# Kernel tuning notes

Hardware: AMD Instinct MI355X
Metric: run time of the kernel (lower is better)

Reference implementation:

```python
import jax, jax.numpy as jnp
import numpy as np

NUM_HEADS = 8
WINDOW = 64
ENCODERS = 6
EPS = 1e-5


def _positional_encoding(S, D, dtype=jnp.float32):
    pos = jnp.arange(S, dtype=jnp.float32)[:, None]
    div = jnp.exp(-jnp.log(10000.0) * jnp.arange(0, D, 2, dtype=jnp.float32) / D)
    ang = pos * div  # [S, D/2]
    pe = jnp.zeros((S, D), dtype=jnp.float32)
    pe = pe.at[:, 0::2].set(jnp.sin(ang)).at[:, 1::2].set(jnp.cos(ang))
    return pe.astype(dtype)


def _layernorm(x, g, b):
    mu = jnp.mean(x, axis=-1, keepdims=True)
    var = jnp.var(x, axis=-1, keepdims=True)
    return (x - mu) * jax.lax.rsqrt(var + EPS) * g + b


def _local_attention(x, wq, bq, wk, bk, wv, bv, window_mask):
    B, S, D = x.shape
    Dh = D // NUM_HEADS
    scale = Dh ** -0.5
    def split(t):  # [B,S,D] -> [B,H,S,Dh]
        return t.reshape(B, S, NUM_HEADS, Dh).transpose(0, 2, 1, 3)
    q = split(x @ wq.T + bq)
    k = split(x @ wk.T + bk)
    v = split(x @ wv.T + bv)
    scores = jnp.einsum('bhqd,bhkd->bhqk', q, k)
    # FAITHFUL: out-of-window entries are ZERO (not -inf); softmax over full S.
    scores = jnp.where(window_mask, scores, 0.0) * scale
    probs = jax.nn.softmax(scores, axis=-1)
    out = jnp.einsum('bhqk,bhkd->bhqd', probs, v)
    return out.transpose(0, 2, 1, 3).reshape(B, S, D)


def reference(inputs, emb, wq, bq, wk, bk, wv, bv, ln_g, ln_b,
              fc1_w, fc1_b, fc2_w, fc2_b, out_w, out_b):
    B, S = inputs.shape
    D = emb.shape[1]
    # window slice in torch source: [max(0, i-W), min(S, i+W))  (end exclusive)
    i = jnp.arange(S)[:, None]
    j = jnp.arange(S)[None, :]
    window_mask = (j >= i - WINDOW) & (j < i + WINDOW)  # [S, S]

    x = emb[inputs]  # [B, S, D]
    x = x + _positional_encoding(S, D, x.dtype)
    for _ in range(ENCODERS):  # shared weights across encoder iterations
        a = _local_attention(x, wq, bq, wk, bk, wv, bv, window_mask)
        x = _layernorm(a, ln_g, ln_b)
        h = jax.nn.relu(x @ fc1_w.T + fc1_b)
        x = (h @ fc2_w.T + fc2_b) + x
        x = _layernorm(x, ln_g, ln_b)
    x = x.reshape(B, S * D)
    return x @ out_w.T + out_b


def setup_inputs() -> dict:
    key = jax.random.key(0)
    ks = jax.random.split(key, 16)
    B, S, D, Hd, V, C = 8, 1024, 512, 2048, 32000, 6
    s = 0.02
    return {
        'inputs': jax.random.randint(ks[0], (B, S), 0, 31999),
        'emb': jax.random.normal(ks[1], (V, D), jnp.float32) * s,
        'wq': jax.random.normal(ks[2], (D, D), jnp.float32) * s,
        'bq': jnp.zeros((D,), jnp.float32),
        'wk': jax.random.normal(ks[3], (D, D), jnp.float32) * s,
        'bk': jnp.zeros((D,), jnp.float32),
        'wv': jax.random.normal(ks[4], (D, D), jnp.float32) * s,
        'bv': jnp.zeros((D,), jnp.float32),
        'ln_g': jnp.ones((D,), jnp.float32),
        'ln_b': jnp.zeros((D,), jnp.float32),
        'fc1_w': jax.random.normal(ks[5], (Hd, D), jnp.float32) * s,
        'fc1_b': jnp.zeros((Hd,), jnp.float32),
        'fc2_w': jax.random.normal(ks[6], (D, Hd), jnp.float32) * s,
        'fc2_b': jnp.zeros((D,), jnp.float32),
        'out_w': jax.random.normal(ks[7], (C, S * D), jnp.float32) * s,
        'out_b': jnp.zeros((C,), jnp.float32),
    }
```

## Files before the change

kernel.cpp:

```cpp
#include <hip/hip_runtime.h>

#define S_LEN 1024
#define DMODEL 512
#define NHEADS 8
#define DHEAD 64
#define HDIM 2048
#define WIN 64

typedef _Float16 f16x8 __attribute__((ext_vector_type(8)));
typedef _Float16 f16x2 __attribute__((ext_vector_type(2)));
typedef float f32x4 __attribute__((ext_vector_type(4)));
typedef float f32x16 __attribute__((ext_vector_type(16)));

__device__ __forceinline__ void stage16(const _Float16* g, _Float16* l) {
  __builtin_amdgcn_global_load_lds((const __attribute__((address_space(1))) unsigned int*)g,
                                   (__attribute__((address_space(3))) unsigned int*)l, 16, 0, 0);
}

__global__ void wprep_kernel(const float* __restrict__ wq, const float* __restrict__ wk,
                             const float* __restrict__ wv, const float* __restrict__ bq,
                             const float* __restrict__ bk, const float* __restrict__ bv,
                             const float* __restrict__ w1, const float* __restrict__ w2,
                             _Float16* __restrict__ Wqkv, float* __restrict__ bqkv,
                             _Float16* __restrict__ W1h, _Float16* __restrict__ W2h) {
  int i = blockIdx.x * 256 + threadIdx.x;
  if (i < 262144) {
    Wqkv[i]          = (_Float16)wq[i];
    Wqkv[262144 + i] = (_Float16)wk[i];
    Wqkv[524288 + i] = (_Float16)wv[i];
  }
  if (i < 1048576) {
    W1h[i] = (_Float16)w1[i];
    W2h[i] = (_Float16)w2[i];
  }
  if (i < 512) { bqkv[i] = bq[i]; bqkv[512 + i] = bk[i]; bqkv[1024 + i] = bv[i]; }
}

__global__ void embed_pe_kernel(const int* __restrict__ inputs, const float* __restrict__ emb,
                                float* __restrict__ X, _Float16* __restrict__ Xb) {
  int row = blockIdx.x;
  int s = row & (S_LEN - 1);
  int t = threadIdx.x;
  int tok = inputs[row];
  float dv = __expf(-logf(10000.0f) * (2.0f * (float)t) / (float)DMODEL);
  float ang = (float)s * dv;
  float sv = sinf(ang);
  float cv = cosf(ang);
  size_t base = (size_t)row * DMODEL + 2 * t;
  float x0 = emb[(size_t)tok * DMODEL + 2 * t] + sv;
  float x1 = emb[(size_t)tok * DMODEL + 2 * t + 1] + cv;
  X[base] = x0; X[base + 1] = x1;
  f16x2 h; h[0] = (_Float16)x0; h[1] = (_Float16)x1;
  *(f16x2*)(Xb + base) = h;
}

#define EPI_PLAIN 0
#define EPI_RELU16 1
#define EPI_RES 2
#define EPI_F16 3

template <int EPI>
__launch_bounds__(256)
__global__ void mfma_gemm(const _Float16* __restrict__ A, const _Float16* __restrict__ W,
                          const float* __restrict__ bias, const float* __restrict__ res,
                          float* __restrict__ Cf, _Float16* __restrict__ Ch,
                          int M, int N, int K) {
  __shared__ _Float16 As[128 * 32];
  __shared__ _Float16 Bs[128 * 32];
  const int bm = blockIdx.x * 128;
  const int bn = blockIdx.y * 128;
  const int t = threadIdx.x;
  const int lane = t & 63;
  const int w = t >> 6;
  const int wr = w >> 1, wc = w & 1;
  const int l15 = lane & 15, l4 = lane >> 4;

  const int idx0 = t, idx1 = t + 256;
  const int r0 = idx0 >> 2, kg0 = (idx0 & 3) << 3;
  const int r1 = idx1 >> 2, kg1 = (idx1 & 3) << 3;
  const _Float16* Ag0 = A + (size_t)(bm + r0) * K + kg0;
  const _Float16* Ag1 = A + (size_t)(bm + r1) * K + kg1;
  const _Float16* Wg0 = W + (size_t)(bn + r0) * K + kg0;
  const _Float16* Wg1 = W + (size_t)(bn + r1) * K + kg1;
  _Float16* Al0 = As + idx0 * 8;
  _Float16* Al1 = As + idx1 * 8;
  _Float16* Bl0 = Bs + idx0 * 8;
  _Float16* Bl1 = Bs + idx1 * 8;

  f32x4 acc[4][4] = {};
  for (int k0 = 0; k0 < K; k0 += 32) {
    stage16(Ag0 + k0, Al0);
    stage16(Ag1 + k0, Al1);
    stage16(Wg0 + k0, Bl0);
    stage16(Wg1 + k0, Bl1);
    __syncthreads();
    f16x8 af[4], bf[4];
#pragma unroll
    for (int m = 0; m < 4; ++m)
      af[m] = *(const f16x8*)&As[(wr * 64 + m * 16 + l15) * 32 + l4 * 8];
#pragma unroll
    for (int n = 0; n < 4; ++n)
      bf[n] = *(const f16x8*)&Bs[(wc * 64 + n * 16 + l15) * 32 + l4 * 8];
#pragma unroll
    for (int m = 0; m < 4; ++m)
#pragma unroll
      for (int n = 0; n < 4; ++n)
        acc[m][n] = __builtin_amdgcn_mfma_f32_16x16x32_f16(af[m], bf[n], acc[m][n], 0, 0, 0);
    __syncthreads();
  }
#pragma unroll
  for (int m = 0; m < 4; ++m) {
    int row = bm + wr * 64 + m * 16 + l4 * 4;
#pragma unroll
    for (int n = 0; n < 4; ++n) {
      int col = bn + wc * 64 + n * 16 + l15;
      float bb = bias[col];
#pragma unroll
      for (int j = 0; j < 4; ++j) {
        float v = acc[m][n][j] + bb;
        if (EPI == EPI_RELU16) {
          v = fmaxf(v, 0.0f);
          Ch[(size_t)(row + j) * N + col] = (_Float16)v;
        } else if (EPI == EPI_F16) {
          Ch[(size_t)(row + j) * N + col] = (_Float16)v;
        } else if (EPI == EPI_RES) {
          Cf[(size_t)(row + j) * N + col] = v + res[(size_t)(row + j) * N + col];
        } else {
          Cf[(size_t)(row + j) * N + col] = v;
        }
      }
    }
  }
}

__global__ void vs_zero_kernel(float* __restrict__ VS) {
  VS[blockIdx.x * 256 + threadIdx.x] = 0.0f;
}
__global__ void vsum_kernel(const _Float16* __restrict__ QKVh, float* __restrict__ VS) {
  int c = threadIdx.x;
  int chunk = blockIdx.x, b = blockIdx.y;
  const _Float16* base = QKVh + ((size_t)(b * S_LEN + chunk * 128)) * 1536 + 1024 + c;
  float acc = 0.f;
  for (int i = 0; i < 128; ++i) acc += (float)base[(size_t)i * 1536];
  atomicAdd(&VS[b * 512 + c], acc);
}

#define KTMAX 256
#define VTS 264

__launch_bounds__(256)
__global__ void attn_kernel(const _Float16* __restrict__ QKVh, const float* __restrict__ VSg,
                            float* __restrict__ O) {
  __shared__ _Float16 Ks[KTMAX * 64];
  __shared__ _Float16 Vt[64 * VTS];
  __shared__ float VsC[8][64];

  const int qb0 = blockIdx.x * 128, h = blockIdx.y, b = blockIdx.z;
  const int jlo = max(0, qb0 - WIN);
  const int jhi = min(S_LEN, qb0 + 128 + WIN);
  const int KT = jhi - jlo;
  const int t = threadIdx.x;
  const int lane = t & 63, w = t >> 6;
  const int hi = lane >> 5, l31 = lane & 31;

  const _Float16* Kg = QKVh + ((size_t)(b * S_LEN + jlo)) * 1536 + 512 + h * 64;
#pragma unroll
  for (int p = 0; p < 8; ++p) {
    int u = t + p * 256;
    int row = u >> 3;
    int cb = (u & 7) * 16;
    int rowc = min(row, KT - 1);
    int scb = cb ^ ((row & 7) << 4);
    stage16(Kg + (size_t)rowc * 1536 + (scb >> 1), Ks + u * 8);
  }
  const _Float16* Vg = QKVh + ((size_t)(b * S_LEN + jlo)) * 1536 + 1024 + h * 64;
#pragma unroll
  for (int p = 0; p < 8; ++p) {
    int u = t + p * 256;
    int row = u >> 3;
    int d0 = (u & 7) * 8;
    f16x8 v = {0, 0, 0, 0, 0, 0, 0, 0};
    if (row < KT) v = *(const f16x8*)(Vg + (size_t)row * 1536 + d0);
#pragma unroll
    for (int e = 0; e < 8; ++e) Vt[(d0 + e) * VTS + row] = v[e];
  }
  __syncthreads();
  for (int slot = t; slot < 512; slot += 256) {
    int c = slot >> 6, d = slot & 63;
    const f16x8* col = (const f16x8*)(Vt + d * VTS + c * 32);
    float s = 0.f;
#pragma unroll
    for (int g = 0; g < 4; ++g) {
      f16x8 v = col[g];
#pragma unroll
      for (int e = 0; e < 8; ++e) s += (float)v[e];
    }
    VsC[c][d] = s;
  }
  const int qw = qb0 + w * 32;
  const _Float16* Qg = QKVh + ((size_t)(b * S_LEN + qw + l31)) * 1536 + h * 64;
  f16x8 qf[4];
#pragma unroll
  for (int ds = 0; ds < 4; ++ds) qf[ds] = *(const f16x8*)(Qg + ds * 16 + hi * 8);
  __syncthreads();

  const int c0 = max(0, qw - WIN - jlo) >> 5;
  const int c1 = min(KT, qw + 96 - jlo) >> 5;
  const int nproc = (c1 - c0) * 32;
  const int i = qw + l31;
  const int wlo = i - WIN, whi = i + WIN;

  float m = 0.f, l = 0.f;
  f32x16 accA = {}, accB = {};

  union PK { f16x2 h; unsigned u; };
  union A8 { unsigned u[4]; f16x8 h; };

  for (int c = c0; c < c1; ++c) {
    const int kb = c * 32;
    f32x16 sf = {};
#pragma unroll
    for (int ds = 0; ds < 4; ++ds) {
      int row = kb + l31;
      int cbyte = ((ds * 16 + hi * 8) * 2) ^ ((row & 7) << 4);
      f16x8 kf = *(const f16x8*)((const char*)Ks + row * 128 + cbyte);
      sf = __builtin_amdgcn_mfma_f32_32x32x16_f16(kf, qf[ds], sf, 0, 0, 0);
    }
    float s[16]; float pm = -1e30f;
#pragma unroll
    for (int r = 0; r < 16; ++r) {
      int gk = jlo + kb + (r & 3) + 8 * (r >> 2) + 4 * hi;
      float v = (gk >= wlo && gk < whi) ? sf[r] * 0.125f : 0.f;
      s[r] = v;
      pm = fmaxf(pm, v);
    }
    pm = fmaxf(pm, __shfl_xor(pm, 32));
    if (!__all(pm <= m + 8.f)) {
      float mn = fmaxf(m, pm);
      float f = __expf(m - mn);
      l *= f;
#pragma unroll
      for (int r = 0; r < 16; ++r) {
        int q = (r & 3) + 8 * (r >> 2) + 4 * hi;
        float fr = __shfl(f, q);
        accA[r] *= fr; accB[r] *= fr;
      }
      m = mn;
    }
    float p[16]; float ls = 0.f;
#pragma unroll
    for (int r = 0; r < 16; ++r) { p[r] = __expf(s[r] - m); ls += p[r]; }
    l += ls;
    unsigned u[8], x[8];
#pragma unroll
    for (int kk = 0; kk < 8; ++kk) {
      PK cv; cv.h[0] = (_Float16)p[2 * kk]; cv.h[1] = (_Float16)p[2 * kk + 1];
      u[kk] = cv.u;
    }
#pragma unroll
    for (int kk = 0; kk < 8; ++kk) x[kk] = (unsigned)__shfl_xor((int)u[kk], 32);
    A8 a0, a1;
    a0.u[0] = hi ? x[2] : u[0]; a0.u[1] = hi ? x[3] : u[1];
    a0.u[2] = hi ? u[2] : x[0]; a0.u[3] = hi ? u[3] : x[1];
    a1.u[0] = hi ? x[6] : u[4]; a1.u[1] = hi ? x[7] : u[5];
    a1.u[2] = hi ? u[6] : x[4]; a1.u[3] = hi ? u[7] : x[5];
#pragma unroll
    for (int ks = 0; ks < 2; ++ks) {
      f16x8 pa = ks ? a1.h : a0.h;
      f16x8 v0 = *(const f16x8*)(Vt + (size_t)(l31) * VTS + kb + ks * 16 + hi * 8);
      f16x8 v1 = *(const f16x8*)(Vt + (size_t)(32 + l31) * VTS + kb + ks * 16 + hi * 8);
      accA = __builtin_amdgcn_mfma_f32_32x32x16_f16(pa, v0, accA, 0, 0, 0);
      accB = __builtin_amdgcn_mfma_f32_32x32x16_f16(pa, v1, accB, 0, 0, 0);
    }
  }

  l = l + __shfl_xor(l, 32);
  const int dA = l31, dB = 32 + l31;
  float vsA = 0.f, vsB = 0.f;
  for (int c = c0; c < c1; ++c) { vsA += VsC[c][dA]; vsB += VsC[c][dB]; }
  const float vtA = VSg[b * 512 + h * 64 + dA];
  const float vtB = VSg[b * 512 + h * 64 + dB];
  const float zcount = (float)(S_LEN - nproc);
#pragma unroll
  for (int r = 0; r < 16; ++r) {
    int q = (r & 3) + 8 * (r >> 2) + 4 * hi;
    float mq = __shfl(m, q);
    float lq = __shfl(l, q);
    float em = __expf(-mq);
    float denom = lq + zcount * em;
    float inv = 1.0f / denom;
    size_t rowbase = ((size_t)(b * S_LEN + qw + q)) * DMODEL + h * 64;
    O[rowbase + dA] = (accA[r] + em * (vtA - vsA)) * inv;
    O[rowbase + dB] = (accB[r] + em * (vtB - vsB)) * inv;
  }
}

__global__ void ln_kernel(const float* __restrict__ X, const float* __restrict__ g,
                          const float* __restrict__ be, float* __restrict__ Y,
                          _Float16* __restrict__ Yh) {
  int row = blockIdx.x;
  int t = threadIdx.x;
  const float* x = X + (size_t)row * DMODEL;
  float2 v = *(const float2*)(x + 2 * t);
  float s = v.x + v.y;
  float sq = v.x * v.x + v.y * v.y;
#pragma unroll
  for (int off = 32; off; off >>= 1) {
    s += __shfl_xor(s, off);
    sq += __shfl_xor(sq, off);
  }
  __shared__ float ss[4], sqq[4];
  int w = t >> 6, lane = t & 63;
  if (lane == 0) { ss[w] = s; sqq[w] = sq; }
  __syncthreads();
  s = ss[0] + ss[1] + ss[2] + ss[3];
  sq = sqq[0] + sqq[1] + sqq[2] + sqq[3];
  float mu = s * (1.0f / DMODEL);
  float var = sq * (1.0f / DMODEL) - mu * mu;
  float rstd = rsqrtf(var + 1e-5f);
  float g0 = g[2 * t], g1 = g[2 * t + 1];
  float b0 = be[2 * t], b1 = be[2 * t + 1];
  float2 o;
  o.x = (v.x - mu) * rstd * g0 + b0;
  o.y = (v.y - mu) * rstd * g1 + b1;
  *(float2*)(Y + (size_t)row * DMODEL + 2 * t) = o;
  f16x2 hh; hh[0] = (_Float16)o.x; hh[1] = (_Float16)o.y;
  *(f16x2*)(Yh + (size_t)row * DMODEL + 2 * t) = hh;
}

__global__ void outproj_partial_kernel(const float* __restrict__ X, const float* __restrict__ Wo,
                                       float* __restrict__ part) {
  const int KTOT = S_LEN * DMODEL;
  const int CH = KTOT / 16;
  int chunk = blockIdx.x, c = blockIdx.y, b = blockIdx.z;
  const float* x = X + (size_t)b * KTOT + (size_t)chunk * CH;
  const float* wv = Wo + (size_t)c * KTOT + (size_t)chunk * CH;
  float acc = 0.f;
  for (int i = threadIdx.x * 4; i < CH; i += 256 * 4) {
    float4 a = *(const float4*)(x + i);
    float4 w4 = *(const float4*)(wv + i);
    acc += a.x * w4.x + a.y * w4.y + a.z * w4.z + a.w * w4.w;
  }
#pragma unroll
  for (int off = 32; off; off >>= 1) acc += __shfl_xor(acc, off);
  __shared__ float red[4];
  int w = threadIdx.x >> 6, lane = threadIdx.x & 63;
  if (lane == 0) red[w] = acc;
  __syncthreads();
  if (threadIdx.x == 0)
    part[(b * 6 + c) * 16 + chunk] = red[0] + red[1] + red[2] + red[3];
}

__global__ void outproj_final_kernel(const float* __restrict__ part, const float* __restrict__ ob,
                                     float* __restrict__ out) {
  int idx = threadIdx.x;
  if (idx < 48) {
    float s = 0.f;
#pragma unroll
    for (int k = 0; k < 16; ++k) s += part[idx * 16 + k];
    out[idx] = s + ob[idx % 6];
  }
}

extern "C" void kernel_launch(void* const* d_in, const int* in_sizes, int n_in,
                              void* d_out, int out_size, void* d_ws, size_t ws_size,
                              hipStream_t stream) {
  (void)in_sizes; (void)n_in; (void)out_size; (void)ws_size;
  const int*   inputs = (const int*)  d_in[0];
  const float* emb    = (const float*)d_in[1];
  const float* wq     = (const float*)d_in[2];
  const float* bq     = (const float*)d_in[3];
  const float* wk     = (const float*)d_in[4];
  const float* bk     = (const float*)d_in[5];
  const float* wv     = (const float*)d_in[6];
  const float* bv     = (const float*)d_in[7];
  const float* ln_g   = (const float*)d_in[8];
  const float* ln_b   = (const float*)d_in[9];
  const float* fc1_w  = (const float*)d_in[10];
  const float* fc1_b  = (const float*)d_in[11];
  const float* fc2_w  = (const float*)d_in[12];
  const float* fc2_b  = (const float*)d_in[13];
  const float* out_w  = (const float*)d_in[14];
  const float* out_b  = (const float*)d_in[15];
  float* out = (float*)d_out;

  const int M = 8192;
  char* p = (char*)d_ws;
  float*    X    = (float*)p;      p += (size_t)M * 512 * 4;
  _Float16* Xb   = (_Float16*)p;   p += (size_t)M * 512 * 2;
  _Float16* QKVh = (_Float16*)p;   p += (size_t)M * 1536 * 2;
  float*    XB   = (float*)p;      p += (size_t)M * 512 * 4;
  _Float16* XBb  = (_Float16*)p;   p += (size_t)M * 512 * 2;
  _Float16* H    = (_Float16*)p;   p += (size_t)M * 2048 * 2;
  float*    Ab   = (float*)H;
  _Float16* Wqkv = (_Float16*)p;   p += (size_t)1536 * 512 * 2;
  _Float16* W1h  = (_Float16*)p;   p += (size_t)2048 * 512 * 2;
  _Float16* W2h  = (_Float16*)p;   p += (size_t)512 * 2048 * 2;
  float*    bqkv = (float*)p;      p += 1536 * 4;
  float*    VS   = (float*)p;      p += 4096 * 4;
  float*    part = (float*)p;      p += 768 * 4;

  wprep_kernel<<<4096, 256, 0, stream>>>(wq, wk, wv, bq, bk, bv, fc1_w, fc2_w,
                                         Wqkv, bqkv, W1h, W2h);
  embed_pe_kernel<<<8192, 256, 0, stream>>>(inputs, emb, X, Xb);
  for (int it = 0; it < 6; ++it) {
    mfma_gemm<EPI_F16><<<dim3(64, 12), 256, 0, stream>>>(Xb, Wqkv, bqkv, nullptr,
                                                         nullptr, QKVh, M, 1536, 512);
    vs_zero_kernel<<<16, 256, 0, stream>>>(VS);
    vsum_kernel<<<dim3(8, 8), 512, 0, stream>>>(QKVh, VS);
    attn_kernel<<<dim3(8, 8, 8), 256, 0, stream>>>(QKVh, VS, Ab);
    ln_kernel<<<8192, 256, 0, stream>>>(Ab, ln_g, ln_b, XB, XBb);
    mfma_gemm<EPI_RELU16><<<dim3(64, 16), 256, 0, stream>>>(XBb, W1h, fc1_b, nullptr,
                                                            nullptr, H, M, 2048, 512);
    mfma_gemm<EPI_RES><<<dim3(64, 4), 256, 0, stream>>>(H, W2h, fc2_b, XB,
                                                        X, nullptr, M, 512, 2048);
    ln_kernel<<<8192, 256, 0, stream>>>(X, ln_g, ln_b, X, Xb);
  }
  outproj_partial_kernel<<<dim3(16, 6, 8), 256, 0, stream>>>(X, out_w, part);
  outproj_final_kernel<<<1, 64, 0, stream>>>(part, out_b, out);
}
```

Before: 891.4 us.

## Use 512-thread GEMM blocks, split-K FC2, and fuse bias+residual into LayerNorm

Each GEMM block now uses 8 waves (512 threads) on the same 128x128 tile, so each wave owns a 32x64 sub-tile and a thread issues one async load per operand instead of two. The FC2 GEMM, which had only 256 blocks, is split along K into two halves written to separate fp32 partial buffers that alias X and the QKV buffer. A new fused LayerNorm kernel sums the partials, bias and residual before normalizing. This targets low occupancy and the long K loop of FC2, at the cost of extra partial-buffer traffic and an extra read in the LayerNorm.

Result: faster. 789.7 us (-11.4%).

```diff
diff --git a/kernel.cpp b/kernel.cpp
--- a/kernel.cpp
+++ b/kernel.cpp
@@ -54,67 +54,62 @@
   *(f16x2*)(Xb + base) = h;
 }
 
-#define EPI_PLAIN 0
 #define EPI_RELU16 1
-#define EPI_RES 2
 #define EPI_F16 3
+#define EPI_PART 4
 
 template <int EPI>
-__launch_bounds__(256)
-__global__ void mfma_gemm(const _Float16* __restrict__ A, const _Float16* __restrict__ W,
-                          const float* __restrict__ bias, const float* __restrict__ res,
-                          float* __restrict__ Cf, _Float16* __restrict__ Ch,
-                          int M, int N, int K) {
+__launch_bounds__(512)
+__global__ void mfma_gemm8(const _Float16* __restrict__ A, const _Float16* __restrict__ W,
+                           const float* __restrict__ bias,
+                           float* __restrict__ Cf0, float* __restrict__ Cf1,
+                           _Float16* __restrict__ Ch,
+                           int M, int N, int Kstride, int Kslice) {
   __shared__ _Float16 As[128 * 32];
   __shared__ _Float16 Bs[128 * 32];
   const int bm = blockIdx.x * 128;
   const int bn = blockIdx.y * 128;
+  const int z = blockIdx.z;
   const int t = threadIdx.x;
   const int lane = t & 63;
   const int w = t >> 6;
   const int wr = w >> 1, wc = w & 1;
   const int l15 = lane & 15, l4 = lane >> 4;
 
-  const int idx0 = t, idx1 = t + 256;
-  const int r0 = idx0 >> 2, kg0 = (idx0 & 3) << 3;
-  const int r1 = idx1 >> 2, kg1 = (idx1 & 3) << 3;
-  const _Float16* Ag0 = A + (size_t)(bm + r0) * K + kg0;
-  const _Float16* Ag1 = A + (size_t)(bm + r1) * K + kg1;
-  const _Float16* Wg0 = W + (size_t)(bn + r0) * K + kg0;
-  const _Float16* Wg1 = W + (size_t)(bn + r1) * K + kg1;
-  _Float16* Al0 = As + idx0 * 8;
-  _Float16* Al1 = As + idx1 * 8;
-  _Float16* Bl0 = Bs + idx0 * 8;
-  _Float16* Bl1 = Bs + idx1 * 8;
-
-  f32x4 acc[4][4] = {};
-  for (int k0 = 0; k0 < K; k0 += 32) {
-    stage16(Ag0 + k0, Al0);
-    stage16(Ag1 + k0, Al1);
-    stage16(Wg0 + k0, Bl0);
-    stage16(Wg1 + k0, Bl1);
+  const int srow = t >> 2, skg = (t & 3) << 3;
+  const _Float16* Ag = A + (size_t)(bm + srow) * Kstride + skg;
+  const _Float16* Wg = W + (size_t)(bn + srow) * Kstride + skg;
+  _Float16* Al = As + t * 8;
+  _Float16* Bl = Bs + t * 8;
+
+  const int kbeg = z * Kslice, kend = kbeg + Kslice;
+  f32x4 acc[2][4] = {};
+  for (int k0 = kbeg; k0 < kend; k0 += 32) {
+    stage16(Ag + k0, Al);
+    stage16(Wg + k0, Bl);
     __syncthreads();
-    f16x8 af[4], bf[4];
-#pragma unroll
-    for (int m = 0; m < 4; ++m)
-      af[m] = *(const f16x8*)&As[(wr * 64 + m * 16 + l15) * 32 + l4 * 8];
+    f16x8 af[2], bf[4];
+#pragma unroll
+    for (int m = 0; m < 2; ++m)
+      af[m] = *(const f16x8*)&As[(wr * 32 + m * 16 + l15) * 32 + l4 * 8];
 #pragma unroll
     for (int n = 0; n < 4; ++n)
       bf[n] = *(const f16x8*)&Bs[(wc * 64 + n * 16 + l15) * 32 + l4 * 8];
 #pragma unroll
-    for (int m = 0; m < 4; ++m)
+    for (int m = 0; m < 2; ++m)
 #pragma unroll
       for (int n = 0; n < 4; ++n)
         acc[m][n] = __builtin_amdgcn_mfma_f32_16x16x32_f16(af[m], bf[n], acc[m][n], 0, 0, 0);
     __syncthreads();
   }
-#pragma unroll
-  for (int m = 0; m < 4; ++m) {
-    int row = bm + wr * 64 + m * 16 + l4 * 4;
+  float* dst = (EPI == EPI_PART) ? (z ? Cf1 : Cf0) : Cf0;
+#pragma unroll
+  for (int m = 0; m < 2; ++m) {
+    int row = bm + wr * 32 + m * 16 + l4 * 4;
 #pragma unroll
     for (int n = 0; n < 4; ++n) {
       int col = bn + wc * 64 + n * 16 + l15;
-      float bb = bias[col];
+      float bb = (EPI == EPI_PART) ? 0.f : bias[col];
 #pragma unroll
       for (int j = 0; j < 4; ++j) {
         float v = acc[m][n][j] + bb;
@@ -123,10 +118,8 @@
           Ch[(size_t)(row + j) * N + col] = (_Float16)v;
         } else if (EPI == EPI_F16) {
           Ch[(size_t)(row + j) * N + col] = (_Float16)v;
-        } else if (EPI == EPI_RES) {
-          Cf[(size_t)(row + j) * N + col] = v + res[(size_t)(row + j) * N + col];
         } else {
-          Cf[(size_t)(row + j) * N + col] = v;
+          dst[(size_t)(row + j) * N + col] = v;
         }
       }
     }
@@ -326,6 +319,45 @@
   *(float2*)(Y + (size_t)row * DMODEL + 2 * t) = o;
   f16x2 hh; hh[0] = (_Float16)o.x; hh[1] = (_Float16)o.y;
   *(f16x2*)(Yh + (size_t)row * DMODEL + 2 * t) = hh;
+}
+
+__global__ void ln2_fused_kernel(const float* __restrict__ P0, const float* __restrict__ P1,
+                                 const float* __restrict__ XB, const float* __restrict__ fb,
+                                 const float* __restrict__ g, const float* __restrict__ be,
+                                 float* __restrict__ Y, _Float16* __restrict__ Yh) {
+  int row = blockIdx.x;
+  int t = threadIdx.x;
+  size_t off = (size_t)row * DMODEL + 2 * t;
+  float2 p0 = *(const float2*)(P0 + off);
+  float2 p1 = *(const float2*)(P1 + off);
+  float2 xb = *(const float2*)(XB + off);
+  float2 v;
+  v.x = p0.x + p1.x + fb[2 * t]     + xb.x;
+  v.y = p0.y + p1.y + fb[2 * t + 1] + xb.y;
+  float s = v.x + v.y;
+  float sq = v.x * v.x + v.y * v.y;
+#pragma unroll
+  for (int off2 = 32; off2; off2 >>= 1) {
+    s += __shfl_xor(s, off2);
+    sq += __shfl_xor(sq, off2);
+  }
+  __shared__ float ss[4], sqq[4];
+  int w = t >> 6, lane = t & 63;
+  if (lane == 0) { ss[w] = s; sqq[w] = sq; }
+  __syncthreads();
+  s = ss[0] + ss[1] + ss[2] + ss[3];
+  sq = sqq[0] + sqq[1] + sqq[2] + sqq[3];
+  float mu = s * (1.0f / DMODEL);
+  float var = sq * (1.0f / DMODEL) - mu * mu;
+  float rstd = rsqrtf(var + 1e-5f);
+  float g0 = g[2 * t], g1 = g[2 * t + 1];
+  float b0 = be[2 * t], b1 = be[2 * t + 1];
+  float2 o;
+  o.x = (v.x - mu) * rstd * g0 + b0;
+  o.y = (v.y - mu) * rstd * g1 + b1;
+  *(float2*)(Y + off) = o;
+  f16x2 hh; hh[0] = (_Float16)o.x; hh[1] = (_Float16)o.y;
+  *(f16x2*)(Yh + off) = hh;
 }
 
 __global__ void outproj_partial_kernel(const float* __restrict__ X, const float* __restrict__ Wo,
@@ -399,22 +431,24 @@
   float*    bqkv = (float*)p;      p += 1536 * 4;
   float*    VS   = (float*)p;      p += 4096 * 4;
   float*    part = (float*)p;      p += 768 * 4;
+  float*    P0   = X;
+  float*    P1   = (float*)QKVh;
 
   wprep_kernel<<<4096, 256, 0, stream>>>(wq, wk, wv, bq, bk, bv, fc1_w, fc2_w,
                                          Wqkv, bqkv, W1h, W2h);
   embed_pe_kernel<<<8192, 256, 0, stream>>>(inputs, emb, X, Xb);
   for (int it = 0; it < 6; ++it) {
-    mfma_gemm<EPI_F16><<<dim3(64, 12), 256, 0, stream>>>(Xb, Wqkv, bqkv, nullptr,
-                                                         nullptr, QKVh, M, 1536, 512);
+    mfma_gemm8<EPI_F16><<<dim3(64, 12), 512, 0, stream>>>(Xb, Wqkv, bqkv, nullptr, nullptr,
+                                                          QKVh, M, 1536, 512, 512);
     vs_zero_kernel<<<16, 256, 0, stream>>>(VS);
     vsum_kernel<<<dim3(8, 8), 512, 0, stream>>>(QKVh, VS);
     attn_kernel<<<dim3(8, 8, 8), 256, 0, stream>>>(QKVh, VS, Ab);
     ln_kernel<<<8192, 256, 0, stream>>>(Ab, ln_g, ln_b, XB, XBb);
-    mfma_gemm<EPI_RELU16><<<dim3(64, 16), 256, 0, stream>>>(XBb, W1h, fc1_b, nullptr,
-                                                            nullptr, H, M, 2048, 512);
-    mfma_gemm<EPI_RES><<<dim3(64, 4), 256, 0, stream>>>(H, W2h, fc2_b, XB,
-                                                        X, nullptr, M, 512, 2048);
-    ln_kernel<<<8192, 256, 0, stream>>>(X, ln_g, ln_b, X, Xb);
+    mfma_gemm8<EPI_RELU16><<<dim3(64, 16), 512, 0, stream>>>(XBb, W1h, fc1_b, nullptr, nullptr,
+                                                             H, M, 2048, 512, 512);
+    mfma_gemm8<EPI_PART><<<dim3(64, 4, 2), 512, 0, stream>>>(H, W2h, nullptr, P0, P1,
+                                                             nullptr, M, 512, 2048, 1024);
+    ln2_fused_kernel<<<8192, 256, 0, stream>>>(P0, P1, XB, fc2_b, ln_g, ln_b, X, Xb);
   }
   outproj_partial_kernel<<<dim3(16, 6, 8), 256, 0, stream>>>(X, out_w, part);
   outproj_final_kernel<<<1, 64, 0, stream>>>(part, out_b, out);
```
